# Optimization experiments

Measured on AMD Instinct MI355X. Metric: run time of the kernel, lower is better.

## Reference

```python
import jax, jax.numpy as jnp
import numpy as np

TOP_K = 8
NUM_EXPERTS = 64
N_TOKENS = 16384
N_EMBED = 4096
EPS = 1e-12  # F.normalize default eps


def setup_inputs() -> dict:
    key = jax.random.key(0)
    k_x, k_wr, k_br, k_wn, k_bn, k_noise = jax.random.split(key, 6)
    scale = 1.0 / np.sqrt(N_EMBED)
    return {
        "x": jax.random.normal(k_x, (N_TOKENS, N_EMBED), dtype=jnp.float32),
        "w_route": jax.random.normal(k_wr, (N_EMBED, NUM_EXPERTS), dtype=jnp.float32) * scale,
        "b_route": jax.random.normal(k_br, (NUM_EXPERTS,), dtype=jnp.float32) * scale,
        "w_noise": jax.random.normal(k_wn, (N_EMBED, NUM_EXPERTS), dtype=jnp.float32) * scale,
        "b_noise": jax.random.normal(k_bn, (NUM_EXPERTS,), dtype=jnp.float32) * scale,
        "noise": jax.random.normal(k_noise, (N_TOKENS, NUM_EXPERTS), dtype=jnp.float32),
    }


def _l1_normalize(v):
    return v / jnp.maximum(jnp.sum(jnp.abs(v)), EPS)


def reference(x, w_route, b_route, w_noise, b_noise, noise):
    # dual linear projections: [N, D] @ [D, E] -> [N, E]
    logits = x @ w_route + b_route
    noise_logits = x @ w_noise + b_noise
    noisy_logits = logits + noise * jax.nn.softplus(noise_logits)

    # top-k (sorted descending, matches torch.topk)
    top_vals, top_idx = jax.lax.top_k(noisy_logits, TOP_K)  # [N, K]
    rows = jnp.arange(noisy_logits.shape[0])[:, None]

    # scatter top-k logits into -inf, softmax -> sparse gate distribution
    sparse_logits = jnp.full_like(noisy_logits, -jnp.inf).at[rows, top_idx].set(top_vals)
    router_output = jax.nn.softmax(sparse_logits, axis=-1)  # [N, E]

    # aux loss (training path). Faithful to torch scatter semantics:
    # gates[n, top_idx[n, j]] = router_output[n, j] (first K columns of src).
    probs = jax.nn.softmax(noisy_logits, axis=-1)
    gates = jnp.zeros_like(probs).at[rows, top_idx].set(router_output[:, :TOP_K])
    probs_sum = probs.sum(0)                                  # [E]
    freq = (gates > 0).astype(jnp.float32).sum(0)             # [E]
    lsesq = jnp.sum(jax.nn.logsumexp(noisy_logits, axis=-1) ** 2)
    switchloss = NUM_EXPERTS * jnp.sum(_l1_normalize(probs_sum) * _l1_normalize(freq))
    zloss = lsesq / noisy_logits.shape[0]
    aux_loss = switchloss + 0.1 * zloss

    return router_output, top_idx, aux_loss
```

## Files before the change

### kernel.cpp

```cpp
#include <hip/hip_runtime.h>
#include <math.h>

#define NT 16384
#define NE 4096
#define NX 64
#define TK 8

#define BM 32
#define NBLK (NT / BM)
#define NSTEP 64

#define RO_SIZE (NT * NX)
#define TI_OFF  RO_SIZE
#define AUX_IDX (RO_SIZE + NT * TK)

#define MAXFLAG 8192
#define PSB_IDX 8256
#define FRB_IDX (PSB_IDX + NBLK * 64)
#define L2B_IDX (FRB_IDX + NBLK * 64)
#define WS_FLOATS (L2B_IDX + NBLK)
#define BPACK_OFF (((WS_FLOATS * 4) + 255) & ~255)
#define BPACK_USHORTS (128 * 4 * 2 * 128 * 8)
#define WS_NEED ((size_t)BPACK_OFF + (size_t)BPACK_USHORTS * 2)

#define DELTA_FP32 5e-5f
#define DELTA_BF16 2.5e-4f

typedef __attribute__((ext_vector_type(8))) short bf16x8_t;
typedef __attribute__((ext_vector_type(4))) float f32x4_t;

__device__ __forceinline__ float neginf() { return __int_as_float(0xff800000); }

__device__ __forceinline__ unsigned short bf16_trunc(float f) {
    return (unsigned short)(__float_as_uint(f) >> 16);
}
__device__ __forceinline__ unsigned short bf16_rtn(float f) {
    unsigned u = __float_as_uint(f);
    unsigned r = u + 0x7fffu + ((u >> 16) & 1u);
    return (unsigned short)(r >> 16);
}
__device__ __forceinline__ float bf16_to_f(unsigned short h) {
    return __uint_as_float(((unsigned)h) << 16);
}

__device__ __forceinline__ void split8(const float4& a, const float4& b,
                                       bf16x8_t& h, bf16x8_t& l) {
    float f[8] = {a.x, a.y, a.z, a.w, b.x, b.y, b.z, b.w};
    #pragma unroll
    for (int j = 0; j < 8; ++j) {
        unsigned short hh = bf16_trunc(f[j]);
        h[j] = (short)hh;
        l[j] = (short)bf16_rtn(f[j] - bf16_to_f(hh));
    }
}

#define GLOAD16(GP, LP) __builtin_amdgcn_global_load_lds(                     \
    (const __attribute__((address_space(1))) void*)(GP),                      \
    (__attribute__((address_space(3))) void*)(LP), 16, 0, 0)

__global__ __launch_bounds__(512) void prep_w_kernel(
    const float* __restrict__ w_route, const float* __restrict__ w_noise,
    unsigned short* __restrict__ bp)
{
    const int kt = blockIdx.x;
    const int t = threadIdx.x;
    const int col = t & 127;
    const int kq = t >> 7;
    const float* src = (col < NX) ? (w_route + col) : (w_noise + (col - NX));
    const int kbase = kt * 32 + kq * 8;
    bf16x8_t h8, l8;
    #pragma unroll
    for (int i = 0; i < 8; ++i) {
        float v = src[(size_t)(kbase + i) * NX];
        unsigned short hh = bf16_trunc(v);
        h8[i] = (short)hh;
        l8[i] = (short)bf16_rtn(v - bf16_to_f(hh));
    }
    unsigned short* base = bp + ((size_t)((kt * 4 + kq) * 2) * 128 + col) * 8;
    *(bf16x8_t*)base = h8;
    *(bf16x8_t*)(base + 128 * 8) = l8;
}

__global__ __launch_bounds__(512, 4) void fused32_kernel(
    const float* __restrict__ x,
    const unsigned short* __restrict__ bp,
    const float* __restrict__ b_route, const float* __restrict__ b_noise,
    const float* __restrict__ noise,
    float* __restrict__ out,
    float* __restrict__ ps_blk, float* __restrict__ fr_blk,
    float* __restrict__ lse2_blk,
    int* __restrict__ flag_cnt, int* __restrict__ flag_list)
{
    __shared__ __align__(16) char ldsraw[81920];

    const int tid = threadIdx.x;
    const int wid = tid >> 6;
    const int lane = tid & 63;
    const int l15 = lane & 15;
    const int kq = lane >> 4;
    const int rg = wid >> 2;
    const int cgq = wid & 3;
    const int bm = blockIdx.x * BM;

    const int sar = tid >> 4;
    const int sac = tid & 15;
    const int sag = sac ^ (sar & 15);
    const float* sA = x + (size_t)(bm + sar) * NE + sag * 4;
    char* dA = ldsraw + tid * 16;
    char* ldsB = ldsraw + 16384;
    char* dB = ldsB + tid * 16;

    #define STAGE(BUF, ST) do {                                               \
        GLOAD16(sA + (ST) * 64, dA + (BUF) * 8192);                           \
        const unsigned short* sB_ = bp + (size_t)(ST) * 16384 + tid * 8;      \
        char* dB_ = dB + (BUF) * 32768;                                       \
        GLOAD16(sB_,         dB_);                                            \
        GLOAD16(sB_ + 4096,  dB_ + 8192);                                     \
        GLOAD16(sB_ + 8192,  dB_ + 16384);                                    \
        GLOAD16(sB_ + 12288, dB_ + 24576);                                    \
    } while (0)

    f32x4_t acc0 = (f32x4_t){0.f, 0.f, 0.f, 0.f};
    f32x4_t acc1 = (f32x4_t){0.f, 0.f, 0.f, 0.f};

    STAGE(0, 0);
    __syncthreads();

    const int arow = rg * 16 + l15;
    const char* aRow = ldsraw + arow * 256;
    const int bBase = (kq * 2) * 128 * 16 + (cgq * 32 + l15) * 16;
    const int bLo   = bBase + 128 * 16;

    for (int st = 0; st < NSTEP; ++st) {
        const int cur = st & 1;
        if (st + 1 < NSTEP) STAGE(cur ^ 1, st + 1);

        const char* aB = aRow + cur * 8192;
        const char* bT = ldsB + cur * 32768;
        #pragma unroll
        for (int sub = 0; sub < 2; ++sub) {
            const int c0 = sub * 8 + kq * 2;
            float4 a0 = *(const float4*)(aB + ((c0 ^ l15) << 4));
            float4 a1 = *(const float4*)(aB + (((c0 + 1) ^ l15) << 4));
            const char* bS = bT + sub * 16384;
            bf16x8_t bh0 = *(const bf16x8_t*)(bS + bBase);
            bf16x8_t bh1 = *(const bf16x8_t*)(bS + bBase + 256);
            bf16x8_t bl0 = *(const bf16x8_t*)(bS + bLo);
            bf16x8_t bl1 = *(const bf16x8_t*)(bS + bLo + 256);
            bf16x8_t ah, al;
            split8(a0, a1, ah, al);
            acc0 = __builtin_amdgcn_mfma_f32_16x16x32_bf16(ah, bh0, acc0, 0, 0, 0);
            acc1 = __builtin_amdgcn_mfma_f32_16x16x32_bf16(ah, bh1, acc1, 0, 0, 0);
            acc0 = __builtin_amdgcn_mfma_f32_16x16x32_bf16(al, bh0, acc0, 0, 0, 0);
            acc1 = __builtin_amdgcn_mfma_f32_16x16x32_bf16(al, bh1, acc1, 0, 0, 0);
            acc0 = __builtin_amdgcn_mfma_f32_16x16x32_bf16(ah, bl0, acc0, 0, 0, 0);
            acc1 = __builtin_amdgcn_mfma_f32_16x16x32_bf16(ah, bl1, acc1, 0, 0, 0);
        }
        __syncthreads();
    }
    #undef STAGE

    float (*part)[130] = (float (*)[130])ldsraw;
    #pragma unroll
    for (int j = 0; j < 4; ++j) {
        int tok = rg * 16 + (lane >> 4) * 4 + j;
        part[tok][cgq * 32 + l15]      = acc0[j];
        part[tok][cgq * 32 + 16 + l15] = acc1[j];
    }
    __syncthreads();

    const float br = b_route[lane];
    const float bnv = b_noise[lane];
    float ps_l = 0.f, fr_l = 0.f, l2_l = 0.f;

    for (int tt = 0; tt < 4; ++tt) {
        const int tok = wid * 4 + tt;
        const int gt  = bm + tok;
        float lr = part[tok][lane] + br;
        float ln = part[tok][64 + lane] + bnv;
        float nz = noise[(size_t)gt * NX + lane];
        float sp = fmaxf(ln, 0.f) + log1pf(expf(-fabsf(ln)));
        float v  = lr + nz * sp;

        float vv = v;
        float tv[9]; int ti[9];
        #pragma unroll
        for (int s = 0; s < 9; ++s) {
            float mv = vv; int mi = lane;
            #pragma unroll
            for (int off = 32; off > 0; off >>= 1) {
                float ov = __shfl_xor(mv, off);
                int   oi = __shfl_xor(mi, off);
                if (ov > mv || (ov == mv && oi < mi)) { mv = ov; mi = oi; }
            }
            tv[s] = mv; ti[s] = mi;
            if (lane == mi) vv = neginf();
        }

        float ming = 1e30f;
        #pragma unroll
        for (int s = 0; s < 8; ++s) ming = fminf(ming, tv[s] - tv[s + 1]);
        if (lane == 0 && ming < DELTA_BF16) {
            int p = atomicAdd(flag_cnt, 1);
            if (p < MAXFLAG) flag_list[p] = gt;
        }

        const float m0 = tv[0];
        float e8[8], s8 = 0.f;
        #pragma unroll
        for (int s = 0; s < 8; ++s) { e8[s] = expf(tv[s] - m0); s8 += e8[s]; }
        float r = 0.f;
        #pragma unroll
        for (int s = 0; s < 8; ++s) if (ti[s] == lane) r = e8[s] / s8;
        out[(size_t)gt * NX + lane] = r;
        if (lane < TK) out[TI_OFF + (size_t)gt * TK + lane] = (float)ti[lane];

        float p = expf(v - m0);
        float s64 = p;
        #pragma unroll
        for (int off = 32; off > 0; off >>= 1) s64 += __shfl_xor(s64, off);
        ps_l += p / s64;
        if (lane == 0) { float lse = m0 + logf(s64); l2_l += lse * lse; }

        unsigned tm8 = 0;
        #pragma unroll
        for (int s = 0; s < 8; ++s) if (ti[s] < TK) tm8 |= (1u << ti[s]);
        #pragma unroll
        for (int s = 0; s < 8; ++s)
            if (ti[s] == lane && ((tm8 >> s) & 1u)) fr_l += 1.f;
    }

    float* sps = (float*)(ldsraw + 20480);
    float* sfr = (float*)(ldsraw + 20480 + 2048);
    float* sl2 = (float*)(ldsraw + 20480 + 4096);
    sps[wid * 64 + lane] = ps_l;
    sfr[wid * 64 + lane] = fr_l;
    if (lane == 0) sl2[wid] = l2_l;
    __syncthreads();
    if (wid == 0) {
        float a = 0.f, b = 0.f;
        #pragma unroll
        for (int w = 0; w < 8; ++w) {
            a += sps[w * 64 + lane];
            b += sfr[w * 64 + lane];
        }
        ps_blk[(size_t)blockIdx.x * 64 + lane] = a;
        fr_blk[(size_t)blockIdx.x * 64 + lane] = b;
        if (lane == 0) {
            float z = 0.f;
            #pragma unroll
            for (int w = 0; w < 8; ++w) z += sl2[w];
            lse2_blk[blockIdx.x] = z;
        }
    }
}

#define FBM 64
#define FBN 128
#define FBK 32
#define XPITCH (FBM + 4)
__global__ __launch_bounds__(256) void fused_router_kernel(
    const float* __restrict__ x,
    const float* __restrict__ w_route, const float* __restrict__ b_route,
    const float* __restrict__ w_noise, const float* __restrict__ b_noise,
    const float* __restrict__ noise,
    float* __restrict__ out,
    float* __restrict__ ps_acc, float* __restrict__ fr_acc,
    float* __restrict__ lse2_acc,
    int* __restrict__ flag_cnt, int* __restrict__ flag_list)
{
    __shared__ float smem[FBM * FBN];
    float* xs  = smem;
    float* wst = smem + FBK * XPITCH;
    const int tid = threadIdx.x;
    const int block_m = blockIdx.x * FBM;
    const int row0 = (tid >> 5) * 8;
    const int col0 = (tid & 31) * 4;
    float acc[8][4];
    #pragma unroll
    for (int i = 0; i < 8; ++i)
        #pragma unroll
        for (int j = 0; j < 4; ++j) acc[i][j] = 0.f;
    float4 px[2], pw[4];
    {
        #pragma unroll
        for (int s = 0; s < 2; ++s) {
            int f = tid + s * 256, r = f >> 3, kqv = f & 7;
            px[s] = *reinterpret_cast<const float4*>(x + (size_t)(block_m + r) * NE + kqv * 4);
        }
        #pragma unroll
        for (int s = 0; s < 4; ++s) {
            int f = tid + s * 256, kk = f >> 5, c4 = (f & 31) * 4;
            const float* src = (c4 < NX) ? (w_route + (size_t)kk * NX + c4)
                                         : (w_noise + (size_t)kk * NX + (c4 - NX));
            pw[s] = *reinterpret_cast<const float4*>(src);
        }
    }
    for (int t = 0; t < NE / FBK; ++t) {
        __syncthreads();
        #pragma unroll
        for (int s = 0; s < 2; ++s) {
            int f = tid + s * 256, r = f >> 3, kqv = f & 7;
            xs[(kqv * 4 + 0) * XPITCH + r] = px[s].x;
            xs[(kqv * 4 + 1) * XPITCH + r] = px[s].y;
            xs[(kqv * 4 + 2) * XPITCH + r] = px[s].z;
            xs[(kqv * 4 + 3) * XPITCH + r] = px[s].w;
        }
        #pragma unroll
        for (int s = 0; s < 4; ++s) {
            int f = tid + s * 256, kk = f >> 5, c4 = (f & 31) * 4;
            *reinterpret_cast<float4*>(&wst[kk * FBN + c4]) = pw[s];
        }
        __syncthreads();
        if (t + 1 < NE / FBK) {
            const int k0 = (t + 1) * FBK;
            #pragma unroll
            for (int s = 0; s < 2; ++s) {
                int f = tid + s * 256, r = f >> 3, kqv = f & 7;
                px[s] = *reinterpret_cast<const float4*>(x + (size_t)(block_m + r) * NE + k0 + kqv * 4);
            }
            #pragma unroll
            for (int s = 0; s < 4; ++s) {
                int f = tid + s * 256, kk = f >> 5, c4 = (f & 31) * 4;
                const float* src = (c4 < NX) ? (w_route + (size_t)(k0 + kk) * NX + c4)
                                             : (w_noise + (size_t)(k0 + kk) * NX + (c4 - NX));
                pw[s] = *reinterpret_cast<const float4*>(src);
            }
        }
        #pragma unroll
        for (int k = 0; k < FBK; ++k) {
            float4 xa = *reinterpret_cast<const float4*>(&xs[k * XPITCH + row0]);
            float4 xb = *reinterpret_cast<const float4*>(&xs[k * XPITCH + row0 + 4]);
            float4 wv = *reinterpret_cast<const float4*>(&wst[k * FBN + col0]);
            float xf[8] = {xa.x, xa.y, xa.z, xa.w, xb.x, xb.y, xb.z, xb.w};
            float wf[4] = {wv.x, wv.y, wv.z, wv.w};
            #pragma unroll
            for (int i = 0; i < 8; ++i)
                #pragma unroll
                for (int j = 0; j < 4; ++j)
                    acc[i][j] = fmaf(xf[i], wf[j], acc[i][j]);
        }
    }
    __syncthreads();
    #pragma unroll
    for (int i = 0; i < 8; ++i) {
        float4 v = make_float4(acc[i][0], acc[i][1], acc[i][2], acc[i][3]);
        *reinterpret_cast<float4*>(&smem[(row0 + i) * FBN + col0]) = v;
    }
    __syncthreads();
    const int wave = tid >> 6;
    const int lane = tid & 63;
    const float br = b_route[lane];
    const float bnv = b_noise[lane];
    float ps_l = 0.f, fr_l = 0.f, l2_l = 0.f;
    for (int tt = 0; tt < FBM / 4; ++tt) {
        const int tok = wave * (FBM / 4) + tt;
        const int gt  = block_m + tok;
        float lr = smem[tok * FBN + lane] + br;
        float ln = smem[tok * FBN + NX + lane] + bnv;
        float nz = noise[(size_t)gt * NX + lane];
        float sp = fmaxf(ln, 0.f) + log1pf(expf(-fabsf(ln)));
        float v  = lr + nz * sp;
        float vv = v;
        float tv[9]; int ti[9];
        #pragma unroll
        for (int s = 0; s < 9; ++s) {
            float mv = vv; int mi = lane;
            #pragma unroll
            for (int off = 32; off > 0; off >>= 1) {
                float ov = __shfl_xor(mv, off);
                int   oi = __shfl_xor(mi, off);
                if (ov > mv || (ov == mv && oi < mi)) { mv = ov; mi = oi; }
            }
            tv[s] = mv; ti[s] = mi;
            if (lane == mi) vv = neginf();
        }
        float ming = 1e30f;
        #pragma unroll
        for (int s = 0; s < 8; ++s) ming = fminf(ming, tv[s] - tv[s + 1]);
        if (lane == 0 && ming < DELTA_FP32) {
            int p = atomicAdd(flag_cnt, 1);
            if (p < MAXFLAG) flag_list[p] = gt;
        }
        const float m0 = tv[0];
        float e8[8], s8 = 0.f;
        #pragma unroll
        for (int s = 0; s < 8; ++s) { e8[s] = expf(tv[s] - m0); s8 += e8[s]; }
        float r = 0.f;
        #pragma unroll
        for (int s = 0; s < 8; ++s) if (ti[s] == lane) r = e8[s] / s8;
        out[(size_t)gt * NX + lane] = r;
        if (lane < TK) out[TI_OFF + (size_t)gt * TK + lane] = (float)ti[lane];
        float p = expf(v - m0);
        float s64 = p;
        #pragma unroll
        for (int off = 32; off > 0; off >>= 1) s64 += __shfl_xor(s64, off);
        ps_l += p / s64;
        if (lane == 0) { float lse = m0 + logf(s64); l2_l += lse * lse; }
        unsigned tm8 = 0;
        #pragma unroll
        for (int s = 0; s < 8; ++s) if (ti[s] < TK) tm8 |= (1u << ti[s]);
        #pragma unroll
        for (int s = 0; s < 8; ++s)
            if (ti[s] == lane && ((tm8 >> s) & 1u)) fr_l += 1.f;
    }
    atomicAdd(&ps_acc[lane], ps_l);
    atomicAdd(&fr_acc[lane], fr_l);
    if (lane == 0) atomicAdd(lse2_acc, l2_l);
}

__global__ __launch_bounds__(256) void refine_kernel(
    const float* __restrict__ x, const float* __restrict__ w_route,
    const float* __restrict__ b_route, const float* __restrict__ w_noise,
    const float* __restrict__ b_noise, const float* __restrict__ noise,
    float* __restrict__ out, const int* __restrict__ flag_cnt,
    const int* __restrict__ flag_list)
{
    __shared__ double red[8][64];
    const int tid = threadIdx.x;
    const int lane = tid & 63, wq = tid >> 6;
    int nf = *flag_cnt; if (nf > MAXFLAG) nf = MAXFLAG;
    for (int fi = blockIdx.x; fi < nf; fi += gridDim.x) {
        const int gt = flag_list[fi];
        const float* xr = x + (size_t)gt * NE + wq * 1024;
        const float* wr = w_route + (size_t)wq * 1024 * NX;
        const float* wn = w_noise + (size_t)wq * 1024 * NX;
        double ar0 = 0, ar1 = 0, an0 = 0, an1 = 0;
        for (int k = 0; k < 1024; k += 2) {
            double x0 = xr[k], x1 = xr[k + 1];
            ar0 += x0 * (double)wr[(size_t)k * NX + lane];
            ar1 += x1 * (double)wr[(size_t)(k + 1) * NX + lane];
            an0 += x0 * (double)wn[(size_t)k * NX + lane];
            an1 += x1 * (double)wn[(size_t)(k + 1) * NX + lane];
        }
        red[wq * 2][lane]     = ar0 + ar1;
        red[wq * 2 + 1][lane] = an0 + an1;
        __syncthreads();
        if (tid < 64) {
            double lr = red[0][lane] + red[2][lane] + red[4][lane] + red[6][lane]
                      + (double)b_route[lane];
            double ln = red[1][lane] + red[3][lane] + red[5][lane] + red[7][lane]
                      + (double)b_noise[lane];
            double nz = (double)noise[(size_t)gt * NX + lane];
            double sp = (ln > 0.0) ? (ln + log1p(exp(-ln))) : log1p(exp(ln));
            double v  = lr + nz * sp;
            double vv = v;
            double tv[8]; int ti[8];
            #pragma unroll
            for (int s = 0; s < 8; ++s) {
                double mv = vv; int mi = lane;
                #pragma unroll
                for (int off = 32; off > 0; off >>= 1) {
                    double ov = __shfl_xor(mv, off);
                    int    oi = __shfl_xor(mi, off);
                    if (ov > mv || (ov == mv && oi < mi)) { mv = ov; mi = oi; }
                }
                tv[s] = mv; ti[s] = mi;
                if (lane == mi) vv = -1.0e300;
            }
            double m0 = tv[0], s8 = 0.0, e8[8];
            #pragma unroll
            for (int s = 0; s < 8; ++s) { e8[s] = exp(tv[s] - m0); s8 += e8[s]; }
            float r = 0.f;
            #pragma unroll
            for (int s = 0; s < 8; ++s) if (ti[s] == lane) r = (float)(e8[s] / s8);
            out[(size_t)gt * NX + lane] = r;
            if (lane < TK) out[TI_OFF + (size_t)gt * TK + lane] = (float)ti[lane];
        }
        __syncthreads();
    }
}

__global__ __launch_bounds__(512) void finalize_kernel(
    const float* __restrict__ ps_blk, const float* __restrict__ fr_blk,
    const float* __restrict__ lse2_blk, float* __restrict__ out)
{
    __shared__ float sps[8][64], sfr[8][64], sl2[512];
    const int t = threadIdx.x;
    const int e = t & 63, g = t >> 6;
    float a = 0.f, b = 0.f;
    for (int blk = g; blk < NBLK; blk += 8) {
        a += ps_blk[(size_t)blk * 64 + e];
        b += fr_blk[(size_t)blk * 64 + e];
    }
    sps[g][e] = a;
    sfr[g][e] = b;
    sl2[t] = lse2_blk[t];
    __syncthreads();
    if (t < 64) {
        float p = 0.f, f = 0.f;
        #pragma unroll
        for (int gg = 0; gg < 8; ++gg) { p += sps[gg][t]; f += sfr[gg][t]; }
        float z = 0.f;
        #pragma unroll
        for (int i = 0; i < 8; ++i) z += sl2[t * 8 + i];
        float sp = p, sf = f, sz = z;
        #pragma unroll
        for (int off = 32; off > 0; off >>= 1) {
            sp += __shfl_xor(sp, off);
            sf += __shfl_xor(sf, off);
            sz += __shfl_xor(sz, off);
        }
        float d = (p / fmaxf(sp, 1e-12f)) * (f / fmaxf(sf, 1e-12f));
        #pragma unroll
        for (int off = 32; off > 0; off >>= 1) d += __shfl_xor(d, off);
        if (t == 0)
            out[AUX_IDX] = 64.f * d + 0.1f * (sz / (float)NT);
    }
}

extern "C" void kernel_launch(void* const* d_in, const int* in_sizes, int n_in,
                              void* d_out, int out_size, void* d_ws, size_t ws_size,
                              hipStream_t stream) {
    const float* x       = (const float*)d_in[0];
    const float* w_route = (const float*)d_in[1];
    const float* b_route = (const float*)d_in[2];
    const float* w_noise = (const float*)d_in[3];
    const float* b_noise = (const float*)d_in[4];
    const float* noise   = (const float*)d_in[5];
    float* out = (float*)d_out;

    float* wsf = (float*)d_ws;
    int* flag_cnt  = (int*)wsf;
    int* flag_list = (int*)(wsf + 1);
    float* ps_blk   = wsf + PSB_IDX;
    float* fr_blk   = wsf + FRB_IDX;
    float* lse2_blk = wsf + L2B_IDX;

    hipMemsetAsync(d_ws, 0, (size_t)(1 + MAXFLAG) * sizeof(int), stream);

    if (ws_size >= WS_NEED) {
        unsigned short* bpack = (unsigned short*)((char*)d_ws + BPACK_OFF);
        prep_w_kernel<<<128, 512, 0, stream>>>(w_route, w_noise, bpack);
        fused32_kernel<<<NBLK, 512, 0, stream>>>(
            x, bpack, b_route, b_noise, noise, out,
            ps_blk, fr_blk, lse2_blk, flag_cnt, flag_list);
    } else {
        hipMemsetAsync(ps_blk, 0,
                       (size_t)(WS_FLOATS - PSB_IDX) * sizeof(float), stream);
        fused_router_kernel<<<NT / FBM, 256, 0, stream>>>(
            x, w_route, b_route, w_noise, b_noise, noise, out,
            ps_blk, fr_blk, lse2_blk, flag_cnt, flag_list);
    }

    refine_kernel<<<1024, 256, 0, stream>>>(
        x, w_route, b_route, w_noise, b_noise, noise, out, flag_cnt, flag_list);

    finalize_kernel<<<1, 512, 0, stream>>>(ps_blk, fr_blk, lse2_blk, out);
}
```

Measured before the change: 207.6 us.

## Split x into bf16 hi/lo once at staging instead of per-wave

The x tile is now loaded from global into registers, split into bf16 high/low parts with byte-permute instructions, and written to LDS already in bf16 form, instead of being copied as fp32 via direct global-to-LDS loads and split after every LDS read. Each element is converted once rather than by every wave that consumes it, and the MFMA operands come straight from LDS. The cost is register-staged global loads for x, which can expose load latency before the LDS write at the end of each step.

```diff
diff --git a/kernel.cpp b/kernel.cpp
--- a/kernel.cpp
+++ b/kernel.cpp
@@ -43,15 +43,19 @@
     return __uint_as_float(((unsigned)h) << 16);
 }
 
-__device__ __forceinline__ void split8(const float4& a, const float4& b,
-                                       bf16x8_t& h, bf16x8_t& l) {
-    float f[8] = {a.x, a.y, a.z, a.w, b.x, b.y, b.z, b.w};
-    #pragma unroll
-    for (int j = 0; j < 8; ++j) {
-        unsigned short hh = bf16_trunc(f[j]);
-        h[j] = (short)hh;
-        l[j] = (short)bf16_rtn(f[j] - bf16_to_f(hh));
-    }
+__device__ __forceinline__ void split4(const float4& f,
+                                       unsigned& h0, unsigned& h1,
+                                       unsigned& l0, unsigned& l1) {
+    unsigned u0 = __float_as_uint(f.x), u1 = __float_as_uint(f.y);
+    unsigned u2 = __float_as_uint(f.z), u3 = __float_as_uint(f.w);
+    h0 = __builtin_amdgcn_perm(u1, u0, 0x07060302u);
+    h1 = __builtin_amdgcn_perm(u3, u2, 0x07060302u);
+    float g0 = f.x - __uint_as_float(u0 & 0xffff0000u);
+    float g1 = f.y - __uint_as_float(u1 & 0xffff0000u);
+    float g2 = f.z - __uint_as_float(u2 & 0xffff0000u);
+    float g3 = f.w - __uint_as_float(u3 & 0xffff0000u);
+    l0 = __builtin_amdgcn_perm(__float_as_uint(g1), __float_as_uint(g0), 0x07060302u);
+    l1 = __builtin_amdgcn_perm(__float_as_uint(g3), __float_as_uint(g2), 0x07060302u);
 }
 
 #define GLOAD16(GP, LP) __builtin_amdgcn_global_load_lds(                     \
@@ -102,16 +106,18 @@
     const int cgq = wid & 3;
     const int bm = blockIdx.x * BM;
 
-    const int sar = tid >> 4;
-    const int sac = tid & 15;
-    const int sag = sac ^ (sar & 15);
-    const float* sA = x + (size_t)(bm + sar) * NE + sag * 4;
-    char* dA = ldsraw + tid * 16;
+    const int srow = tid >> 4;
+    const int sq = tid & 15;
+    const int skc = sq >> 1;
+    const int shalf = sq & 1;
+    const int srl = srow & 15;
+    const int offA = srow * 256 + ((skc ^ srl) << 4) + shalf * 8;
+    const float* sxa = x + (size_t)(bm + srow) * NE + sq * 4;
+
     char* ldsB = ldsraw + 16384;
     char* dB = ldsB + tid * 16;
 
-    #define STAGE(BUF, ST) do {                                               \
-        GLOAD16(sA + (ST) * 64, dA + (BUF) * 8192);                           \
+    #define STAGE_B(BUF, ST) do {                                             \
         const unsigned short* sB_ = bp + (size_t)(ST) * 16384 + tid * 8;      \
         char* dB_ = dB + (BUF) * 32768;                                       \
         GLOAD16(sB_,         dB_);                                            \
@@ -120,35 +126,47 @@
         GLOAD16(sB_ + 12288, dB_ + 24576);                                    \
     } while (0)
 
+    #define WRITE_A(BUF) do {                                                 \
+        unsigned h0_, h1_, l0_, l1_;                                          \
+        split4(rx, h0_, h1_, l0_, l1_);                                       \
+        const int ob_ = (BUF) * 8192;                                         \
+        *(int2*)(ldsraw + ob_ + offA)         = make_int2((int)h0_, (int)h1_);\
+        *(int2*)(ldsraw + ob_ + (offA ^ 128)) = make_int2((int)l0_, (int)l1_);\
+    } while (0)
+
     f32x4_t acc0 = (f32x4_t){0.f, 0.f, 0.f, 0.f};
     f32x4_t acc1 = (f32x4_t){0.f, 0.f, 0.f, 0.f};
 
-    STAGE(0, 0);
+    float4 rx = *(const float4*)(sxa);
+    STAGE_B(0, 0);
+    WRITE_A(0);
     __syncthreads();
 
-    const int arow = rg * 16 + l15;
-    const char* aRow = ldsraw + arow * 256;
-    const int bBase = (kq * 2) * 128 * 16 + (cgq * 32 + l15) * 16;
-    const int bLo   = bBase + 128 * 16;
+    const char* aRow = ldsraw + (rg * 16 + l15) * 256;
+    const int rl = l15;
+    const int bBase = kq * 4096 + (cgq * 32 + l15) * 16;
+    const int bLo   = bBase + 2048;
 
     for (int st = 0; st < NSTEP; ++st) {
         const int cur = st & 1;
-        if (st + 1 < NSTEP) STAGE(cur ^ 1, st + 1);
+        if (st + 1 < NSTEP) {
+            rx = *(const float4*)(sxa + (st + 1) * 64);
+            STAGE_B(cur ^ 1, st + 1);
+        }
 
         const char* aB = aRow + cur * 8192;
         const char* bT = ldsB + cur * 32768;
         #pragma unroll
         for (int sub = 0; sub < 2; ++sub) {
-            const int c0 = sub * 8 + kq * 2;
-            float4 a0 = *(const float4*)(aB + ((c0 ^ l15) << 4));
-            float4 a1 = *(const float4*)(aB + (((c0 + 1) ^ l15) << 4));
+            const int kcr = sub * 4 + kq;
+            const int ch = (kcr ^ rl) << 4;
+            bf16x8_t ah = *(const bf16x8_t*)(aB + ch);
+            bf16x8_t al = *(const bf16x8_t*)(aB + (ch ^ 128));
             const char* bS = bT + sub * 16384;
             bf16x8_t bh0 = *(const bf16x8_t*)(bS + bBase);
             bf16x8_t bh1 = *(const bf16x8_t*)(bS + bBase + 256);
             bf16x8_t bl0 = *(const bf16x8_t*)(bS + bLo);
             bf16x8_t bl1 = *(const bf16x8_t*)(bS + bLo + 256);
-            bf16x8_t ah, al;
-            split8(a0, a1, ah, al);
             acc0 = __builtin_amdgcn_mfma_f32_16x16x32_bf16(ah, bh0, acc0, 0, 0, 0);
             acc1 = __builtin_amdgcn_mfma_f32_16x16x32_bf16(ah, bh1, acc1, 0, 0, 0);
             acc0 = __builtin_amdgcn_mfma_f32_16x16x32_bf16(al, bh0, acc0, 0, 0, 0);
@@ -156,9 +174,12 @@
             acc0 = __builtin_amdgcn_mfma_f32_16x16x32_bf16(ah, bl0, acc0, 0, 0, 0);
             acc1 = __builtin_amdgcn_mfma_f32_16x16x32_bf16(ah, bl1, acc1, 0, 0, 0);
         }
+
+        if (st + 1 < NSTEP) WRITE_A(cur ^ 1);
         __syncthreads();
     }
-    #undef STAGE
+    #undef STAGE_B
+    #undef WRITE_A
 
     float (*part)[130] = (float (*)[130])ldsraw;
     #pragma unroll
```

After: 199.5 us. -3.9%, faster.
